# Kernel tuning notes

Measured on AMD Instinct MI355X. Metric: run time of the kernel, lower is better.

The kernel has to match this reference:

```python
import jax, jax.numpy as jnp
import numpy as np

N_NODES = 10000
N_EDGES = 128000


def _edge_conv(x, row, col, edge_attr, w1, b1, w2, b2):
    # gather endpoints, concat edge features, 2-layer MLP per edge
    m = jnp.concatenate([x[row], x[col], edge_attr], axis=1)  # [E, 2*in+edge]
    m = jax.nn.relu(m @ w1 + b1) @ w2 + b2                    # [E, out]
    # scatter-mean onto source nodes (flow='target_to_source' -> aggregate on row)
    n = x.shape[0]
    s = jax.ops.segment_sum(m, row, num_segments=n)
    cnt = jax.ops.segment_sum(jnp.ones((row.shape[0], 1), m.dtype), row, num_segments=n)
    out = s / jnp.maximum(cnt, 1.0)
    return out, m


def setup_inputs() -> dict:
    key = jax.random.key(0)
    ks = jax.random.split(key, 24)
    f = jnp.float32

    def lin(kw, kb, fan_in, fan_out):
        lim = 1.0 / np.sqrt(fan_in)
        w = jax.random.uniform(kw, (fan_in, fan_out), f, -lim, lim)
        b = jax.random.uniform(kb, (fan_out,), f, -lim, lim)
        return w, b

    inp = {}
    inp['x_org'] = jax.random.normal(ks[0], (N_NODES, 256), f)
    inp['x_rot'] = jax.random.normal(ks[1], (N_NODES, 4), f)
    inp['edge_index'] = jax.random.randint(ks[2], (2, N_EDGES), 0, N_NODES, jnp.int64 if jax.config.jax_enable_x64 else jnp.int32)
    inp['edge_attr'] = jax.random.normal(ks[3], (N_EDGES, 640), f)
    inp['edge_rot'] = jax.random.normal(ks[4], (N_EDGES, 4), f)

    # conv1: Linear(2*260+644=1164, 64), Linear(64, 64)
    inp['c1_w1'], inp['c1_b1'] = lin(ks[5], ks[6], 1164, 64)
    inp['c1_w2'], inp['c1_b2'] = lin(ks[7], ks[8], 64, 64)
    # conv2: Linear(2*64+704=832, 64), Linear(64, 64)
    inp['c2_w1'], inp['c2_b1'] = lin(ks[9], ks[10], 832, 64)
    inp['c2_w2'], inp['c2_b2'] = lin(ks[11], ks[12], 64, 64)
    # conv3: Linear(2*128+128=384, 64), Linear(64, 64)
    inp['c3_w1'], inp['c3_b1'] = lin(ks[13], ks[14], 384, 64)
    inp['c3_w2'], inp['c3_b2'] = lin(ks[15], ks[16], 64, 64)
    # conv4: Linear(384, 64), Linear(64, 64)
    inp['c4_w1'], inp['c4_b1'] = lin(ks[17], ks[18], 384, 64)
    inp['c4_w2'], inp['c4_b2'] = lin(ks[19], ks[20], 64, 64)
    # lin1: Linear(64, 4)
    inp['lin1_w'], inp['lin1_b'] = lin(ks[21], ks[22], 64, 4)
    # edge_fc: Linear(64, 32) -> ReLU -> Linear(32, 1)
    k23 = jax.random.split(ks[23], 4)
    inp['efc_w1'], inp['efc_b1'] = lin(k23[0], k23[1], 64, 32)
    inp['efc_w2'], inp['efc_b2'] = lin(k23[2], k23[3], 32, 1)
    return inp


def reference(x_org, x_rot, edge_index, edge_attr, edge_rot,
              c1_w1, c1_b1, c1_w2, c1_b2,
              c2_w1, c2_b1, c2_w2, c2_b2,
              c3_w1, c3_b1, c3_w2, c3_b2,
              c4_w1, c4_b1, c4_w2, c4_b2,
              lin1_w, lin1_b, efc_w1, efc_b1, efc_w2, efc_b2):
    node_feat = jnp.concatenate([x_org, x_rot], axis=1)
    edge_feat = jnp.concatenate([edge_attr, edge_rot], axis=1)
    row, col = edge_index[0], edge_index[1]
    E = edge_index.shape[1]

    x1, edge_x1 = _edge_conv(node_feat, row, col, edge_feat, c1_w1, c1_b1, c1_w2, c1_b2)
    edge_x1 = jax.nn.relu(edge_x1)

    x2, edge_x2 = _edge_conv(x1, row, col, jnp.concatenate([edge_attr, edge_x1], axis=1),
                             c2_w1, c2_b1, c2_w2, c2_b2)
    x2 = jax.nn.relu(x2)
    edge_x2 = jax.nn.relu(edge_x2)

    x3, edge_x3 = _edge_conv(jnp.concatenate([x2, x1], axis=1), row, col,
                             jnp.concatenate([edge_x2, edge_x1], axis=1),
                             c3_w1, c3_b1, c3_w2, c3_b2)
    x3 = jax.nn.relu(x3)
    edge_x3 = jax.nn.relu(edge_x3)

    x4, edge_x4 = _edge_conv(jnp.concatenate([x3, x2], axis=1), row, col,
                             jnp.concatenate([edge_x3, edge_x2], axis=1),
                             c4_w1, c4_b1, c4_w2, c4_b2)
    x4 = jax.nn.relu(x4)

    x = x4 @ lin1_w + lin1_b  # [N, 4]
    h = edge_x4[: E // 2] + edge_x4[E // 2:]
    pred_edge_res = jax.nn.relu(h @ efc_w1 + efc_b1) @ efc_w2 + efc_b2  # [E/2, 1]

    # F.normalize(x, p=2, dim=1)
    x = x / jnp.maximum(jnp.linalg.norm(x, axis=1, keepdims=True), 1e-12)
    return x, pred_edge_res
```

## Files before the change

### kernel.cpp

```cpp
#include <hip/hip_runtime.h>
#include <stdint.h>


#define N_NODES 10000
#define N_EDGES 128000
#define E_HALF  64000

typedef unsigned short u16;
constexpr int PAD = 18;

using bf16x8 = __attribute__((ext_vector_type(8))) short;
using f32x4  = __attribute__((ext_vector_type(4))) float;

#define MFMA16(A, B, C) C = __builtin_amdgcn_mfma_f32_16x16x32_bf16(A, B, C, 0, 0, 0)

__device__ __align__(256) float g_acc[N_NODES * 64];
__device__ __align__(256) float g_deg[N_NODES];
__device__ __align__(256) float g_P[N_NODES * 128];
__device__ __align__(256) float g_x1[N_NODES * 64];
__device__ __align__(256) float g_x2[N_NODES * 64];
__device__ __align__(256) float g_x3[N_NODES * 64];
__device__ __align__(256) float g_exA[(size_t)N_EDGES * 64];
__device__ __align__(256) float g_exB[(size_t)N_EDGES * 64];
__device__ __align__(256) u16  g_wpA_hi[11 * 4096];
__device__ __align__(256) u16  g_wpA_lo[11 * 4096];
__device__ __align__(256) u16  g_wp2_hi[4096];
__device__ __align__(256) u16  g_wp2_lo[4096];
__device__ __align__(256) int g_row[N_EDGES];
__device__ __align__(256) int g_col[N_EDGES];
__device__ int g_mode;
__device__ int g_is64;

__device__ __forceinline__ float b2f(u16 u) {
    return __uint_as_float(((unsigned int)u) << 16);
}
__device__ __forceinline__ u16 f2b(float f) {
    unsigned int u = __float_as_uint(f);
    u += 0x7FFFu + ((u >> 16) & 1u);
    return (u16)(u >> 16);
}
__device__ __forceinline__ float ldf(const u16* p)   { return b2f(*p); }
__device__ __forceinline__ float ldf(const float* p) { return *p; }
__device__ __forceinline__ void  stf(u16* p, float v)   { *p = f2b(v); }
__device__ __forceinline__ void  stf(float* p, float v) { *p = v; }

__device__ __forceinline__ float4 load4(const float* p) { return *(const float4*)p; }
__device__ __forceinline__ float4 load4(const u16* p) {
    ushort4 v = *(const ushort4*)p;
    return make_float4(b2f(v.x), b2f(v.y), b2f(v.z), b2f(v.w));
}

__device__ __forceinline__ void split_pack(float4 v, uint2& hi, uint2& lo) {
    unsigned int ux = __float_as_uint(v.x), uy = __float_as_uint(v.y);
    unsigned int uz = __float_as_uint(v.z), uw = __float_as_uint(v.w);
    unsigned int hx = ux & 0xFFFF0000u, hy = uy & 0xFFFF0000u;
    unsigned int hz = uz & 0xFFFF0000u, hw = uw & 0xFFFF0000u;
    hi.x = (hx >> 16) | hy;
    hi.y = (hz >> 16) | hw;
    u16 lx = f2b(v.x - __uint_as_float(hx));
    u16 ly = f2b(v.y - __uint_as_float(hy));
    u16 lz = f2b(v.z - __uint_as_float(hz));
    u16 lw = f2b(v.w - __uint_as_float(hw));
    lo.x = (unsigned int)lx | ((unsigned int)ly << 16);
    lo.y = (unsigned int)lz | ((unsigned int)lw << 16);
}

template<int K1, int K2> struct NGOff;
template<> struct NGOff<256, 4> { static constexpr size_t hi = (size_t)260 * 64; };
template<> struct NGOff<64, 0>  { static constexpr size_t hi = (size_t)64 * 64; };
template<> struct NGOff<64, 64> { static constexpr size_t hi = (size_t)128 * 64; };

template<int D>
__device__ __forceinline__ void stage_row(const u16* src, float* sm, int koff, int e, int t) {
    static_assert(D % 4 == 0, "D%4");
    for (int k = t * 4; k < D; k += 1024) {
        ushort4 v = *(const ushort4*)(src + k);
        sm[(koff + k + 0) * PAD + e] = b2f(v.x);
        sm[(koff + k + 1) * PAD + e] = b2f(v.y);
        sm[(koff + k + 2) * PAD + e] = b2f(v.z);
        sm[(koff + k + 3) * PAD + e] = b2f(v.w);
    }
}
template<int D>
__device__ __forceinline__ void stage_row(const float* src, float* sm, int koff, int e, int t) {
    static_assert(D % 4 == 0, "D%4");
    for (int k = t * 4; k < D; k += 1024) {
        float4 v = *(const float4*)(src + k);
        sm[(koff + k + 0) * PAD + e] = v.x;
        sm[(koff + k + 1) * PAD + e] = v.y;
        sm[(koff + k + 2) * PAD + e] = v.z;
        sm[(koff + k + 3) * PAD + e] = v.w;
    }
}

__global__ void detect_kernel(const void* x_org_v, const int* __restrict__ eidx) {
    const u16* w = (const u16*)x_org_v;
    const int t = threadIdx.x;
    int ok = 0;
    for (int i = t; i < 128; i += 64) {
        u16 v = w[i];
        int ex = (v >> 7) & 0xFF;
        ok += ((ex >= 0x68 && ex <= 0x88) || ((v & 0x7FFFu) == 0)) ? 1 : 0;
    }
    #pragma unroll
    for (int off = 32; off >= 1; off >>= 1) ok += __shfl_xor(ok, off);
    bool allz = true;
    for (int i = t; i < 2048; i += 64) allz = allz && (eidx[2 * i + 1] == 0);
    unsigned long long m = __ballot(allz);
    if (t == 0) {
        g_mode = (ok >= 110) ? 0 : 1;
        g_is64 = (m == ~0ull) ? 1 : 0;
    }
}

__global__ void cvt_idx(const int* __restrict__ eidx) {
    const int e = blockIdx.x * 256 + threadIdx.x;
    if (g_is64) {
        g_row[e] = eidx[2 * e];
        g_col[e] = eidx[2 * (e + N_EDGES)];
    } else {
        g_row[e] = eidx[e];
        g_col[e] = eidx[e + N_EDGES];
    }
}

__global__ void zero_all() {
    const int i = blockIdx.x * 256 + threadIdx.x;
    g_acc[i] = 0.f;
    if (i < N_NODES) g_deg[i] = 0.f;
}

__global__ void deg_kernel() {
    const int e = blockIdx.x * 256 + threadIdx.x;
    if (e < N_EDGES) atomicAdd(&g_deg[g_row[e]], 1.0f);
}

template<int K1, typename TA1, int K2, typename TA2, typename TW>
__device__ void node_gemm_body(float* sm, const TA1* A1, const TA2* A2,
                               const TW* Wbase, float* P) {
    constexpr int K = K1 + K2;
    const TW* Blo = Wbase;
    const TW* Bhi = Wbase + NGOff<K1, K2>::hi;
    const int t = threadIdx.x;
    const int c = t & 127;
    const int g = t >> 7;
    const int r0 = blockIdx.x * 16;
    for (int e = 0; e < 16; ++e) {
        stage_row<K1>(A1 + (size_t)(r0 + e) * K1, sm, 0, e, t);
        if constexpr (K2 > 0)
            stage_row<K2>(A2 + (size_t)(r0 + e) * K2, sm, K1, e, t);
    }
    __syncthreads();
    float acc[16];
    #pragma unroll
    for (int e = 0; e < 16; ++e) acc[e] = 0.f;
    const TW* Bp = (c < 64) ? (Blo + c) : (Bhi + (c - 64));
    const int kb = g * (K / 2), ke = kb + K / 2;
    for (int k = kb; k < ke; ++k) {
        float w = ldf(Bp + (size_t)k * 64);
        #pragma unroll
        for (int e = 0; e < 16; ++e) acc[e] += sm[k * PAD + e] * w;
    }
    __syncthreads();
    #pragma unroll
    for (int e = 0; e < 16; ++e) sm[(g * 16 + e) * 128 + c] = acc[e];
    __syncthreads();
    #pragma unroll
    for (int j = 0; j < 8; ++j) {
        int e = g * 8 + j;
        P[(size_t)(r0 + e) * 128 + c] = sm[e * 128 + c] + sm[(16 + e) * 128 + c];
    }
}

template<int K1, int K2>
__global__ void __launch_bounds__(256) node_gemm_in(
        const void* A1, const void* A2, const void* W, float* __restrict__ P) {
    extern __shared__ float sm[];
    if (g_mode == 0)
        node_gemm_body<K1, u16, K2, u16, u16>(sm, (const u16*)A1, (const u16*)A2,
                                              (const u16*)W, P);
    else
        node_gemm_body<K1, float, K2, float, float>(sm, (const float*)A1,
                                              (const float*)A2, (const float*)W, P);
}

template<int K1, int K2>
__global__ void __launch_bounds__(256) node_gemm_ws(
        const float* A1, const float* A2, const void* W, float* __restrict__ P) {
    extern __shared__ float sm[];
    if (g_mode == 0)
        node_gemm_body<K1, float, K2, float, u16>(sm, A1, A2, (const u16*)W, P);
    else
        node_gemm_body<K1, float, K2, float, float>(sm, A1, A2, (const float*)W, P);
}

template<typename TW>
__device__ void pack_w_body(const TW* w1, const TW* w2, int we, int ns) {
    const int idx = blockIdx.x * 256 + threadIdx.x;
    const int t1 = ns * 4096;
    if (idx < t1) {
        const int s = idx >> 12;
        const int rem = idx & 4095;
        const int kt = rem >> 11, ct = (rem >> 9) & 3, l = (rem >> 3) & 63, r = rem & 7;
        const int k = s * 64 + kt * 32 + 4 * (l >> 4) + (r & 3) + 16 * (r >> 2);
        const float v = ldf(w1 + (size_t)(we + k) * 64 + ct * 16 + (l & 15));
        const u16 hh = f2b(v);
        g_wpA_hi[idx] = hh;
        g_wpA_lo[idx] = f2b(v - b2f(hh));
    } else if (idx < t1 + 4096) {
        const int rem = idx - t1;
        const int kt = rem >> 11, ct = (rem >> 9) & 3, l = (rem >> 3) & 63, r = rem & 7;
        const int k = kt * 32 + 4 * (l >> 4) + (r & 3) + 16 * (r >> 2);
        const float v = ldf(w2 + (size_t)k * 64 + ct * 16 + (l & 15));
        const u16 hh = f2b(v);
        g_wp2_hi[rem] = hh;
        g_wp2_lo[rem] = f2b(v - b2f(hh));
    }
}
__global__ void pack_w_k(const void* w1, const void* w2, int we, int ns) {
    if (g_mode == 0) pack_w_body<u16>((const u16*)w1, (const u16*)w2, we, ns);
    else             pack_w_body<float>((const float*)w1, (const float*)w2, we, ns);
}

template<typename TA, typename TW, int NSA, int DB, bool RELU_OUT>
__device__ __forceinline__ void edge_mfma_body(
        u16* smA, int* srow, int* scol, float* b1s, float* b2s,
        float* rot, float* wtl,
        const TA* efa, const float* efb, const TA* rotsrc,
        const TW* w1, const TW* b1v, const TW* b2v, float* eout, int we) {
    constexpr int NS_TOT = NSA + (DB == 64 ? 1 : 0);
    const int t = threadIdx.x;
    const int lane = t & 63, wid = t >> 6;
    const int q = lane >> 4, n = lane & 15;
    const int e0 = blockIdx.x * 128;

    if (t < 128) srow[t] = g_row[e0 + t];
    else         scol[t - 128] = g_col[e0 + t - 128];
    if (t >= 128 && t < 192) b1s[t - 128] = ldf(b1v + (t - 128));
    if (t >= 192)            b2s[t - 192] = ldf(b2v + (t - 192));
    if constexpr (DB == 4) {
        if (t < 128) {
            float4 r4 = load4(rotsrc + (size_t)(e0 + t) * 4);
            rot[t * 4 + 0] = r4.x; rot[t * 4 + 1] = r4.y;
            rot[t * 4 + 2] = r4.z; rot[t * 4 + 3] = r4.w;
        }
        wtl[t] = ldf(w1 + (size_t)(we + NSA * 64 + (t >> 6)) * 64 + (t & 63));
    }

    f32x4 acc[2][4];
    #pragma unroll
    for (int a_ = 0; a_ < 2; ++a_)
        #pragma unroll
        for (int b_ = 0; b_ < 4; ++b_)
            acc[a_][b_] = (f32x4){0.f, 0.f, 0.f, 0.f};

    const int eb = t >> 4;
    const int cc = t & 15;

    for (int s = 0; s < NS_TOT; ++s) {
        #pragma unroll
        for (int p = 0; p < 8; ++p) {
            const int e = p * 16 + eb;
            float4 v;
            if (s < NSA) v = load4(efa + (size_t)(e0 + e) * (NSA * 64) + s * 64 + cc * 4);
            else         v = load4(efb + (size_t)(e0 + e) * 64 + cc * 4);
            uint2 hi, lo; split_pack(v, hi, lo);
            const int elem = (((cc >> 3) * 8 + (e >> 4)) * 64 + (cc & 3) * 16 + (e & 15)) * 8
                           + ((cc >> 2) & 1) * 4;
            *(uint2*)&smA[elem]        = hi;
            *(uint2*)&smA[elem + 8192] = lo;
        }
        __syncthreads();
        const u16* wph = g_wpA_hi + s * 4096;
        const u16* wpl = g_wpA_lo + s * 4096;
        #pragma unroll
        for (int kt = 0; kt < 2; ++kt) {
            const int r0 = ((kt * 8 + wid * 2 + 0) * 64 + lane) * 8;
            const int r1 = ((kt * 8 + wid * 2 + 1) * 64 + lane) * 8;
            bf16x8 ah0 = *(const bf16x8*)&smA[r0];
            bf16x8 ah1 = *(const bf16x8*)&smA[r1];
            bf16x8 al0 = *(const bf16x8*)&smA[r0 + 8192];
            bf16x8 al1 = *(const bf16x8*)&smA[r1 + 8192];
            #pragma unroll
            for (int ct = 0; ct < 4; ++ct) {
                bf16x8 bh = *(const bf16x8*)&wph[(kt * 4 + ct) * 512 + lane * 8];
                bf16x8 bl = *(const bf16x8*)&wpl[(kt * 4 + ct) * 512 + lane * 8];
                MFMA16(ah0, bh, acc[0][ct]);
                MFMA16(ah1, bh, acc[1][ct]);
                MFMA16(al0, bh, acc[0][ct]);
                MFMA16(al1, bh, acc[1][ct]);
                MFMA16(ah0, bl, acc[0][ct]);
                MFMA16(ah1, bl, acc[1][ct]);
            }
        }
        __syncthreads();
    }

    #pragma unroll
    for (int rt = 0; rt < 2; ++rt) {
        #pragma unroll
        for (int ct = 0; ct < 4; ++ct) {
            #pragma unroll
            for (int i = 0; i < 4; ++i) {
                const int rl = wid * 32 + rt * 16 + 4 * q + i;
                const int col = ct * 16 + n;
                float v = acc[rt][ct][i] + b1s[col]
                        + g_P[(size_t)srow[rl] * 128 + col]
                        + g_P[(size_t)scol[rl] * 128 + 64 + col];
                if constexpr (DB == 4) {
                    v += rot[rl * 4 + 0] * wtl[0 * 64 + col]
                       + rot[rl * 4 + 1] * wtl[1 * 64 + col]
                       + rot[rl * 4 + 2] * wtl[2 * 64 + col]
                       + rot[rl * 4 + 3] * wtl[3 * 64 + col];
                }
                v = fmaxf(v, 0.f);
                unsigned int hb = __float_as_uint(v) & 0xFFFF0000u;
                const u16 hh = (u16)(hb >> 16);
                const u16 hl = f2b(v - __uint_as_float(hb));
                const int off = wid * 4096
                              + (((ct >> 1) * 2 + rt) * 64 + (n >> 2) * 16 + 4 * q + i) * 8
                              + (ct & 1) * 4 + (n & 3);
                smA[off]        = hh;
                smA[off + 2048] = hl;
            }
        }
    }

    f32x4 oacc[2][4];
    #pragma unroll
    for (int rt = 0; rt < 2; ++rt)
        #pragma unroll
        for (int ct = 0; ct < 4; ++ct) {
            const float bb = b2s[ct * 16 + n];
            oacc[rt][ct] = (f32x4){bb, bb, bb, bb};
        }
    #pragma unroll
    for (int kt = 0; kt < 2; ++kt) {
        const int r0 = wid * 4096 + ((kt * 2 + 0) * 64 + lane) * 8;
        const int r1 = wid * 4096 + ((kt * 2 + 1) * 64 + lane) * 8;
        bf16x8 ah0 = *(const bf16x8*)&smA[r0];
        bf16x8 ah1 = *(const bf16x8*)&smA[r1];
        bf16x8 al0 = *(const bf16x8*)&smA[r0 + 2048];
        bf16x8 al1 = *(const bf16x8*)&smA[r1 + 2048];
        #pragma unroll
        for (int ct = 0; ct < 4; ++ct) {
            bf16x8 bh = *(const bf16x8*)&g_wp2_hi[(kt * 4 + ct) * 512 + lane * 8];
            bf16x8 bl = *(const bf16x8*)&g_wp2_lo[(kt * 4 + ct) * 512 + lane * 8];
            MFMA16(ah0, bh, oacc[0][ct]);
            MFMA16(ah1, bh, oacc[1][ct]);
            MFMA16(al0, bh, oacc[0][ct]);
            MFMA16(al1, bh, oacc[1][ct]);
            MFMA16(ah0, bl, oacc[0][ct]);
            MFMA16(ah1, bl, oacc[1][ct]);
        }
    }

    #pragma unroll
    for (int rt = 0; rt < 2; ++rt) {
        #pragma unroll
        for (int ct = 0; ct < 4; ++ct) {
            #pragma unroll
            for (int i = 0; i < 4; ++i) {
                const int rl = wid * 32 + rt * 16 + 4 * q + i;
                const int col = ct * 16 + n;
                const float v = oacc[rt][ct][i];
                atomicAdd(&g_acc[(size_t)srow[rl] * 64 + col], v);
                eout[(size_t)(e0 + rl) * 64 + col] = RELU_OUT ? fmaxf(v, 0.f) : v;
            }
        }
    }
}

template<int NSA, int DB, bool RELU_OUT>
__global__ void __launch_bounds__(256, 4) edge_mfma_in(
        const void* efa, const float* efb, const void* rotsrc,
        const void* w1, const void* b1, const void* b2, float* eout, int we) {
    __shared__ u16 smA[16384];
    __shared__ int srow[128], scol[128];
    __shared__ float b1s[64], b2s[64], rot[512], wtl[256];
    if (g_mode == 0)
        edge_mfma_body<u16, u16, NSA, DB, RELU_OUT>(smA, srow, scol, b1s, b2s, rot, wtl,
            (const u16*)efa, efb, (const u16*)rotsrc,
            (const u16*)w1, (const u16*)b1, (const u16*)b2, eout, we);
    else
        edge_mfma_body<float, float, NSA, DB, RELU_OUT>(smA, srow, scol, b1s, b2s, rot, wtl,
            (const float*)efa, efb, (const float*)rotsrc,
            (const float*)w1, (const float*)b1, (const float*)b2, eout, we);
}

template<int NSA, int DB, bool RELU_OUT>
__global__ void __launch_bounds__(256, 4) edge_mfma_ws(
        const float* efa, const float* efb,
        const void* w1, const void* b1, const void* b2, float* eout, int we) {
    __shared__ u16 smA[16384];
    __shared__ int srow[128], scol[128];
    __shared__ float b1s[64], b2s[64], rot[512], wtl[256];
    if (g_mode == 0)
        edge_mfma_body<float, u16, NSA, DB, RELU_OUT>(smA, srow, scol, b1s, b2s, rot, wtl,
            efa, efb, (const float*)nullptr,
            (const u16*)w1, (const u16*)b1, (const u16*)b2, eout, we);
    else
        edge_mfma_body<float, float, NSA, DB, RELU_OUT>(smA, srow, scol, b1s, b2s, rot, wtl,
            efa, efb, (const float*)nullptr,
            (const float*)w1, (const float*)b1, (const float*)b2, eout, we);
}

template<bool RELU>
__global__ void finalize_k(float* __restrict__ dst) {
    const int idx = blockIdx.x * 256 + threadIdx.x;
    float v = g_acc[idx] / fmaxf(g_deg[idx >> 6], 1.0f);
    g_acc[idx] = 0.f;
    if (RELU) v = fmaxf(v, 0.f);
    dst[idx] = v;
}

template<typename T>
__device__ void final_node_body(const T* w, const T* b, T* out) {
    const int t = threadIdx.x;
    const int lane = t & 63;
    const int n = blockIdx.x * 4 + (t >> 6);
    float inv = 1.0f / fmaxf(g_deg[n], 1.0f);
    float x4 = fmaxf(g_acc[(size_t)n * 64 + lane] * inv, 0.0f);
    float r[4];
    #pragma unroll
    for (int j = 0; j < 4; ++j) {
        float v = x4 * ldf(w + lane * 4 + j);
        #pragma unroll
        for (int off = 32; off >= 1; off >>= 1) v += __shfl_xor(v, off);
        r[j] = v + ldf(b + j);
    }
    float nrm = sqrtf(r[0]*r[0] + r[1]*r[1] + r[2]*r[2] + r[3]*r[3]);
    float dn = fmaxf(nrm, 1e-12f);
    if (lane < 4) stf(out + n * 4 + lane, r[lane] / dn);
}
__global__ void final_node(const void* w, const void* b, void* out) {
    if (g_mode == 0) final_node_body<u16>((const u16*)w, (const u16*)b, (u16*)out);
    else             final_node_body<float>((const float*)w, (const float*)b, (float*)out);
}

template<typename T>
__device__ void edge_head_body(const float* ex4, const T* w1, const T* b1,
                               const T* w2, const T* b2, T* out) {
    __shared__ float lw1[2048];
    __shared__ float lw2[32];
    const int t = threadIdx.x;
    for (int i = t; i < 2048; i += 256) lw1[i] = ldf(w1 + i);
    if (t < 32) lw2[t] = ldf(w2 + t);
    __syncthreads();
    const int e = blockIdx.x * 256 + t;
    float a[32];
    #pragma unroll
    for (int j = 0; j < 32; ++j) a[j] = ldf(b1 + j);
    const float* p0 = ex4 + (size_t)e * 64;
    const float* p1 = ex4 + (size_t)(e + E_HALF) * 64;
    for (int c = 0; c < 64; ++c) {
        float h = p0[c] + p1[c];
        #pragma unroll
        for (int j = 0; j < 32; ++j) a[j] += h * lw1[c * 32 + j];
    }
    float s = ldf(b2);
    #pragma unroll
    for (int j = 0; j < 32; ++j) s += fmaxf(a[j], 0.f) * lw2[j];
    stf(out + e, s);
}
__global__ void __launch_bounds__(256) edge_head(const float* ex4,
        const void* w1, const void* b1, const void* w2, const void* b2,
        void* out) {
    if (g_mode == 0)
        edge_head_body<u16>(ex4, (const u16*)w1, (const u16*)b1,
                            (const u16*)w2, (const u16*)b2, (u16*)out + 40000);
    else
        edge_head_body<float>(ex4, (const float*)w1, (const float*)b1,
                              (const float*)w2, (const float*)b2, (float*)out + 40000);
}

__global__ void sentinel_fill(unsigned int* out, int n_words) {
    int i = blockIdx.x * 256 + threadIdx.x;
    if (i < n_words) out[i] = 0x44794479u;
}

static void* sym_addr(const void* symbol) {
    void* p = nullptr;
    (void)hipGetSymbolAddress(&p, symbol);
    return p;
}

extern "C" void kernel_launch(void* const* d_in, const int* in_sizes, int n_in,
                              void* d_out, int out_size, void* d_ws, size_t ws_size,
                              hipStream_t stream) {
    (void)d_ws; (void)ws_size;
    bool ok = (n_in == 27) && (out_size == 104000)
           && (in_sizes[0] == 2560000) && (in_sizes[2] == 256000)
           && (in_sizes[3] == 81920000) && (in_sizes[5] == 74496)
           && (in_sizes[21] == 256) && (in_sizes[25] == 32);
    if (!ok) {
        sentinel_fill<<<204, 256, 0, stream>>>((unsigned int*)d_out, 52000);
        return;
    }
    const void* x_org     = d_in[0];
    const void* x_rot     = d_in[1];
    const int*  eidx      = (const int*)d_in[2];
    const void* edge_attr = d_in[3];
    const void* edge_rot  = d_in[4];

    float* P   = (float*)sym_addr(HIP_SYMBOL(g_P));
    float* x1  = (float*)sym_addr(HIP_SYMBOL(g_x1));
    float* x2  = (float*)sym_addr(HIP_SYMBOL(g_x2));
    float* x3  = (float*)sym_addr(HIP_SYMBOL(g_x3));
    float* exA = (float*)sym_addr(HIP_SYMBOL(g_exA));
    float* exB = (float*)sym_addr(HIP_SYMBOL(g_exB));

    detect_kernel<<<1, 64, 0, stream>>>(x_org, eidx);
    cvt_idx<<<500, 256, 0, stream>>>(eidx);
    zero_all<<<2500, 256, 0, stream>>>();
    deg_kernel<<<500, 256, 0, stream>>>();

    node_gemm_in<256, 4><<<625, 256, 18720, stream>>>(x_org, x_rot, d_in[5], P);
    pack_w_k<<<176, 256, 0, stream>>>(d_in[5], d_in[7], 520, 10);
    edge_mfma_in<10, 4, true><<<1000, 256, 0, stream>>>(
        edge_attr, nullptr, edge_rot, d_in[5], d_in[6], d_in[8], exA, 520);
    finalize_k<false><<<2500, 256, 0, stream>>>(x1);

    node_gemm_ws<64, 0><<<625, 256, 16384, stream>>>(x1, (const float*)nullptr,
                                                     d_in[9], P);
    pack_w_k<<<192, 256, 0, stream>>>(d_in[9], d_in[11], 128, 11);
    edge_mfma_in<10, 64, true><<<1000, 256, 0, stream>>>(
        edge_attr, exA, nullptr, d_in[9], d_in[10], d_in[12], exB, 128);
    finalize_k<true><<<2500, 256, 0, stream>>>(x2);

    node_gemm_ws<64, 64><<<625, 256, 16384, stream>>>(x2, x1, d_in[13], P);
    pack_w_k<<<48, 256, 0, stream>>>(d_in[13], d_in[15], 256, 2);
    edge_mfma_ws<1, 64, true><<<1000, 256, 0, stream>>>(
        exB, exA, d_in[13], d_in[14], d_in[16], exA, 256);
    finalize_k<true><<<2500, 256, 0, stream>>>(x3);

    node_gemm_ws<64, 64><<<625, 256, 16384, stream>>>(x3, x2, d_in[17], P);
    pack_w_k<<<48, 256, 0, stream>>>(d_in[17], d_in[19], 256, 2);
    edge_mfma_ws<1, 64, false><<<1000, 256, 0, stream>>>(
        exA, exB, d_in[17], d_in[18], d_in[20], exB, 256);

    final_node<<<2500, 256, 0, stream>>>(d_in[21], d_in[22], d_out);
    edge_head<<<250, 256, 0, stream>>>(exB, d_in[23], d_in[24], d_in[25], d_in[26],
                                       d_out);
}
```

Baseline: 969.4 us.

## Move node GEMMs to split-bf16 MFMA and swizzle edge LDS layout

Replaces the scalar FP32 per-node projection GEMM with an MFMA kernel that splits the activations and weights into hi/lo bf16 halves, using weights pre-packed by an extended pack kernel. The 4-wide rotation tail is handled in a small FP32 epilogue. It also applies an XOR swizzle to the shared-memory A tiles in both the node and edge MFMA kernels to reduce LDS bank conflicts. In exchange it adds a larger weight-packing pass and three-term bf16 precision emulation.

```diff
diff --git a/kernel.cpp b/kernel.cpp
--- a/kernel.cpp
+++ b/kernel.cpp
@@ -7,7 +7,6 @@
 #define E_HALF  64000
 
 typedef unsigned short u16;
-constexpr int PAD = 18;
 
 using bf16x8 = __attribute__((ext_vector_type(8))) short;
 using f32x4  = __attribute__((ext_vector_type(4))) float;
@@ -26,6 +25,8 @@
 __device__ __align__(256) u16  g_wpA_lo[11 * 4096];
 __device__ __align__(256) u16  g_wp2_hi[4096];
 __device__ __align__(256) u16  g_wp2_lo[4096];
+__device__ __align__(256) u16  g_wnp_hi[4 * 8192];
+__device__ __align__(256) u16  g_wnp_lo[4 * 8192];
 __device__ __align__(256) int g_row[N_EDGES];
 __device__ __align__(256) int g_col[N_EDGES];
 __device__ int g_mode;
@@ -48,6 +49,11 @@
 __device__ __forceinline__ float4 load4(const u16* p) {
     ushort4 v = *(const ushort4*)p;
     return make_float4(b2f(v.x), b2f(v.y), b2f(v.z), b2f(v.w));
+}
+
+template<int KTB>
+__device__ __forceinline__ int swz(int b) {
+    return b ^ ((b >> 4) & 3) ^ (((b >> KTB) & 1) << 2);
 }
 
 __device__ __forceinline__ void split_pack(float4 v, uint2& hi, uint2& lo) {
@@ -65,34 +71,6 @@
     lo.y = (unsigned int)lz | ((unsigned int)lw << 16);
 }
 
-template<int K1, int K2> struct NGOff;
-template<> struct NGOff<256, 4> { static constexpr size_t hi = (size_t)260 * 64; };
-template<> struct NGOff<64, 0>  { static constexpr size_t hi = (size_t)64 * 64; };
-template<> struct NGOff<64, 64> { static constexpr size_t hi = (size_t)128 * 64; };
-
-template<int D>
-__device__ __forceinline__ void stage_row(const u16* src, float* sm, int koff, int e, int t) {
-    static_assert(D % 4 == 0, "D%4");
-    for (int k = t * 4; k < D; k += 1024) {
-        ushort4 v = *(const ushort4*)(src + k);
-        sm[(koff + k + 0) * PAD + e] = b2f(v.x);
-        sm[(koff + k + 1) * PAD + e] = b2f(v.y);
-        sm[(koff + k + 2) * PAD + e] = b2f(v.z);
-        sm[(koff + k + 3) * PAD + e] = b2f(v.w);
-    }
-}
-template<int D>
-__device__ __forceinline__ void stage_row(const float* src, float* sm, int koff, int e, int t) {
-    static_assert(D % 4 == 0, "D%4");
-    for (int k = t * 4; k < D; k += 1024) {
-        float4 v = *(const float4*)(src + k);
-        sm[(koff + k + 0) * PAD + e] = v.x;
-        sm[(koff + k + 1) * PAD + e] = v.y;
-        sm[(koff + k + 2) * PAD + e] = v.z;
-        sm[(koff + k + 3) * PAD + e] = v.w;
-    }
-}
-
 __global__ void detect_kernel(const void* x_org_v, const int* __restrict__ eidx) {
     const u16* w = (const u16*)x_org_v;
     const int t = threadIdx.x;
@@ -135,67 +113,9 @@
     if (e < N_EDGES) atomicAdd(&g_deg[g_row[e]], 1.0f);
 }
 
-template<int K1, typename TA1, int K2, typename TA2, typename TW>
-__device__ void node_gemm_body(float* sm, const TA1* A1, const TA2* A2,
-                               const TW* Wbase, float* P) {
-    constexpr int K = K1 + K2;
-    const TW* Blo = Wbase;
-    const TW* Bhi = Wbase + NGOff<K1, K2>::hi;
-    const int t = threadIdx.x;
-    const int c = t & 127;
-    const int g = t >> 7;
-    const int r0 = blockIdx.x * 16;
-    for (int e = 0; e < 16; ++e) {
-        stage_row<K1>(A1 + (size_t)(r0 + e) * K1, sm, 0, e, t);
-        if constexpr (K2 > 0)
-            stage_row<K2>(A2 + (size_t)(r0 + e) * K2, sm, K1, e, t);
-    }
-    __syncthreads();
-    float acc[16];
-    #pragma unroll
-    for (int e = 0; e < 16; ++e) acc[e] = 0.f;
-    const TW* Bp = (c < 64) ? (Blo + c) : (Bhi + (c - 64));
-    const int kb = g * (K / 2), ke = kb + K / 2;
-    for (int k = kb; k < ke; ++k) {
-        float w = ldf(Bp + (size_t)k * 64);
-        #pragma unroll
-        for (int e = 0; e < 16; ++e) acc[e] += sm[k * PAD + e] * w;
-    }
-    __syncthreads();
-    #pragma unroll
-    for (int e = 0; e < 16; ++e) sm[(g * 16 + e) * 128 + c] = acc[e];
-    __syncthreads();
-    #pragma unroll
-    for (int j = 0; j < 8; ++j) {
-        int e = g * 8 + j;
-        P[(size_t)(r0 + e) * 128 + c] = sm[e * 128 + c] + sm[(16 + e) * 128 + c];
-    }
-}
-
-template<int K1, int K2>
-__global__ void __launch_bounds__(256) node_gemm_in(
-        const void* A1, const void* A2, const void* W, float* __restrict__ P) {
-    extern __shared__ float sm[];
-    if (g_mode == 0)
-        node_gemm_body<K1, u16, K2, u16, u16>(sm, (const u16*)A1, (const u16*)A2,
-                                              (const u16*)W, P);
-    else
-        node_gemm_body<K1, float, K2, float, float>(sm, (const float*)A1,
-                                              (const float*)A2, (const float*)W, P);
-}
-
-template<int K1, int K2>
-__global__ void __launch_bounds__(256) node_gemm_ws(
-        const float* A1, const float* A2, const void* W, float* __restrict__ P) {
-    extern __shared__ float sm[];
-    if (g_mode == 0)
-        node_gemm_body<K1, float, K2, float, u16>(sm, A1, A2, (const u16*)W, P);
-    else
-        node_gemm_body<K1, float, K2, float, float>(sm, A1, A2, (const float*)W, P);
-}
-
 template<typename TW>
-__device__ void pack_w_body(const TW* w1, const TW* w2, int we, int ns) {
+__device__ void pack_w_body(const TW* w1, const TW* w2, int we, int ns,
+                            int hioff, int nsn) {
     const int idx = blockIdx.x * 256 + threadIdx.x;
     const int t1 = ns * 4096;
     if (idx < t1) {
@@ -215,11 +135,130 @@
         const u16 hh = f2b(v);
         g_wp2_hi[rem] = hh;
         g_wp2_lo[rem] = f2b(v - b2f(hh));
-    }
-}
-__global__ void pack_w_k(const void* w1, const void* w2, int we, int ns) {
-    if (g_mode == 0) pack_w_body<u16>((const u16*)w1, (const u16*)w2, we, ns);
-    else             pack_w_body<float>((const float*)w1, (const float*)w2, we, ns);
+    } else if (idx < t1 + 4096 + nsn * 8192) {
+        const int rem = idx - t1 - 4096;
+        const int s = rem >> 13;
+        const int kt = (rem >> 12) & 1, ct = (rem >> 9) & 7, l = (rem >> 3) & 63, r = rem & 7;
+        const int k = s * 64 + kt * 32 + 4 * (l >> 4) + (r & 3) + 16 * (r >> 2);
+        const int col = ct * 16 + (l & 15);
+        const int row = (col < 64) ? k : (hioff + k);
+        const float v = ldf(w1 + (size_t)row * 64 + (col & 63));
+        const u16 hh = f2b(v);
+        g_wnp_hi[rem] = hh;
+        g_wnp_lo[rem] = f2b(v - b2f(hh));
+    }
+}
+__global__ void pack_w_k(const void* w1, const void* w2, int we, int ns,
+                         int hioff, int nsn) {
+    if (g_mode == 0) pack_w_body<u16>((const u16*)w1, (const u16*)w2, we, ns, hioff, nsn);
+    else             pack_w_body<float>((const float*)w1, (const float*)w2, we, ns, hioff, nsn);
+}
+
+template<typename TA, int NS1, int NS2, bool TAIL>
+__device__ void node_mfma_body(u16* smA, float* smrot, float* smwt,
+        const TA* A1, const float* A2, const TA* rotsrc, const TA* w1, float* P) {
+    constexpr int NS = NS1 + NS2;
+    const int t = threadIdx.x;
+    const int lane = t & 63, wid = t >> 6;
+    const int q = lane >> 4, n = lane & 15;
+    const int r0b = blockIdx.x * 64;
+
+    if constexpr (TAIL) {
+        if (t < 64) {
+            const int rr = min(r0b + t, N_NODES - 1);
+            float4 v = load4(rotsrc + (size_t)rr * 4);
+            smrot[t * 4 + 0] = v.x; smrot[t * 4 + 1] = v.y;
+            smrot[t * 4 + 2] = v.z; smrot[t * 4 + 3] = v.w;
+        }
+        for (int i = t; i < 512; i += 256) {
+            const int j = i >> 7, c = i & 127;
+            const int row = (c < 64) ? (256 + j) : (516 + j);
+            smwt[i] = ldf(w1 + (size_t)row * 64 + (c & 63));
+        }
+    }
+
+    f32x4 acc[8];
+    #pragma unroll
+    for (int ct = 0; ct < 8; ++ct) acc[ct] = (f32x4){0.f, 0.f, 0.f, 0.f};
+
+    const int eb = t >> 4;
+    const int cc = t & 15;
+
+    for (int s = 0; s < NS; ++s) {
+        #pragma unroll
+        for (int p = 0; p < 4; ++p) {
+            const int e = p * 16 + eb;
+            const int row = min(r0b + e, N_NODES - 1);
+            float4 v;
+            if constexpr (NS2 > 0)
+                v = (s < NS1) ? load4(A1 + (size_t)row * (NS1 * 64) + s * 64 + cc * 4)
+                              : load4(A2 + (size_t)row * (NS2 * 64) + (s - NS1) * 64 + cc * 4);
+            else
+                v = load4(A1 + (size_t)row * (NS1 * 64) + s * 64 + cc * 4);
+            uint2 hi, lo; split_pack(v, hi, lo);
+            const int blk = ((cc >> 3) * 4 + (e >> 4)) * 64 + (cc & 3) * 16 + (e & 15);
+            const int elem = swz<8>(blk) * 8 + ((cc >> 2) & 1) * 4;
+            *(uint2*)&smA[elem]        = hi;
+            *(uint2*)&smA[elem + 4096] = lo;
+        }
+        __syncthreads();
+        const u16* wph = g_wnp_hi + s * 8192;
+        const u16* wpl = g_wnp_lo + s * 8192;
+        #pragma unroll
+        for (int kt = 0; kt < 2; ++kt) {
+            const int ad = swz<8>((kt * 4 + wid) * 64 + lane) * 8;
+            bf16x8 ah = *(const bf16x8*)&smA[ad];
+            bf16x8 al = *(const bf16x8*)&smA[ad + 4096];
+            #pragma unroll
+            for (int ct = 0; ct < 8; ++ct) {
+                bf16x8 bh = *(const bf16x8*)&wph[(kt * 8 + ct) * 512 + lane * 8];
+                bf16x8 bl = *(const bf16x8*)&wpl[(kt * 8 + ct) * 512 + lane * 8];
+                MFMA16(ah, bh, acc[ct]);
+                MFMA16(al, bh, acc[ct]);
+                MFMA16(ah, bl, acc[ct]);
+            }
+        }
+        __syncthreads();
+    }
+
+    #pragma unroll
+    for (int ct = 0; ct < 8; ++ct) {
+        #pragma unroll
+        for (int i = 0; i < 4; ++i) {
+            const int rl = wid * 16 + 4 * q + i;
+            const int row = r0b + rl;
+            const int col = ct * 16 + n;
+            float v = acc[ct][i];
+            if constexpr (TAIL)
+                v += smrot[rl * 4 + 0] * smwt[0 * 128 + col]
+                   + smrot[rl * 4 + 1] * smwt[1 * 128 + col]
+                   + smrot[rl * 4 + 2] * smwt[2 * 128 + col]
+                   + smrot[rl * 4 + 3] * smwt[3 * 128 + col];
+            if (row < N_NODES) P[(size_t)row * 128 + col] = v;
+        }
+    }
+}
+
+template<int NS1, bool TAIL>
+__global__ void __launch_bounds__(256) node_mfma_in(
+        const void* A1, const void* rotsrc, const void* w1, float* __restrict__ P) {
+    __shared__ u16 smA[8192];
+    __shared__ float smrot[256], smwt[512];
+    if (g_mode == 0)
+        node_mfma_body<u16, NS1, 0, TAIL>(smA, smrot, smwt, (const u16*)A1,
+            nullptr, (const u16*)rotsrc, (const u16*)w1, P);
+    else
+        node_mfma_body<float, NS1, 0, TAIL>(smA, smrot, smwt, (const float*)A1,
+            nullptr, (const float*)rotsrc, (const float*)w1, P);
+}
+
+template<int NS1, int NS2>
+__global__ void __launch_bounds__(256) node_mfma_ws(
+        const float* A1, const float* A2, float* __restrict__ P) {
+    __shared__ u16 smA[8192];
+    __shared__ float smrot[256], smwt[512];
+    node_mfma_body<float, NS1, NS2, false>(smA, smrot, smwt, A1, A2,
+        (const float*)nullptr, (const float*)nullptr, P);
 }
 
 template<typename TA, typename TW, int NSA, int DB, bool RELU_OUT>
@@ -265,8 +304,8 @@
             if (s < NSA) v = load4(efa + (size_t)(e0 + e) * (NSA * 64) + s * 64 + cc * 4);
             else         v = load4(efb + (size_t)(e0 + e) * 64 + cc * 4);
             uint2 hi, lo; split_pack(v, hi, lo);
-            const int elem = (((cc >> 3) * 8 + (e >> 4)) * 64 + (cc & 3) * 16 + (e & 15)) * 8
-                           + ((cc >> 2) & 1) * 4;
+            const int blk = ((cc >> 3) * 8 + (e >> 4)) * 64 + (cc & 3) * 16 + (e & 15);
+            const int elem = swz<9>(blk) * 8 + ((cc >> 2) & 1) * 4;
             *(uint2*)&smA[elem]        = hi;
             *(uint2*)&smA[elem + 8192] = lo;
         }
@@ -275,8 +314,10 @@
         const u16* wpl = g_wpA_lo + s * 4096;
         #pragma unroll
         for (int kt = 0; kt < 2; ++kt) {
-            const int r0 = ((kt * 8 + wid * 2 + 0) * 64 + lane) * 8;
-            const int r1 = ((kt * 8 + wid * 2 + 1) * 64 + lane) * 8;
+            const int b0 = (kt * 8 + wid * 2 + 0) * 64 + lane;
+            const int b1 = (kt * 8 + wid * 2 + 1) * 64 + lane;
+            const int r0 = swz<9>(b0) * 8;
+            const int r1 = swz<9>(b1) * 8;
             bf16x8 ah0 = *(const bf16x8*)&smA[r0];
             bf16x8 ah1 = *(const bf16x8*)&smA[r1];
             bf16x8 al0 = *(const bf16x8*)&smA[r0 + 8192];
@@ -515,27 +556,26 @@
     zero_all<<<2500, 256, 0, stream>>>();
     deg_kernel<<<500, 256, 0, stream>>>();
 
-    node_gemm_in<256, 4><<<625, 256, 18720, stream>>>(x_org, x_rot, d_in[5], P);
-    pack_w_k<<<176, 256, 0, stream>>>(d_in[5], d_in[7], 520, 10);
+    pack_w_k<<<304, 256, 0, stream>>>(d_in[5], d_in[7], 520, 10, 260, 4);
+    node_mfma_in<4, true><<<157, 256, 0, stream>>>(x_org, x_rot, d_in[5], P);
     edge_mfma_in<10, 4, true><<<1000, 256, 0, stream>>>(
         edge_attr, nullptr, edge_rot, d_in[5], d_in[6], d_in[8], exA, 520);
     finalize_k<false><<<2500, 256, 0, stream>>>(x1);
 
-    node_gemm_ws<64, 0><<<625, 256, 16384, stream>>>(x1, (const float*)nullptr,
-                                                     d_in[9], P);
-    pack_w_k<<<192, 256, 0, stream>>>(d_in[9], d_in[11], 128, 11);
+    pack_w_k<<<224, 256, 0, stream>>>(d_in[9], d_in[11], 128, 11, 64, 1);
+    node_mfma_ws<1, 0><<<157, 256, 0, stream>>>(x1, nullptr, P);
     edge_mfma_in<10, 64, true><<<1000, 256, 0, stream>>>(
         edge_attr, exA, nullptr, d_in[9], d_in[10], d_in[12], exB, 128);
     finalize_k<true><<<2500, 256, 0, stream>>>(x2);
 
-    node_gemm_ws<64, 64><<<625, 256, 16384, stream>>>(x2, x1, d_in[13], P);
-    pack_w_k<<<48, 256, 0, stream>>>(d_in[13], d_in[15], 256, 2);
+    pack_w_k<<<112, 256, 0, stream>>>(d_in[13], d_in[15], 256, 2, 128, 2);
+    node_mfma_ws<1, 1><<<157, 256, 0, stream>>>(x2, x1, P);
     edge_mfma_ws<1, 64, true><<<1000, 256, 0, stream>>>(
         exB, exA, d_in[13], d_in[14], d_in[16], exA, 256);
     finalize_k<true><<<2500, 256, 0, stream>>>(x3);
 
-    node_gemm_ws<64, 64><<<625, 256, 16384, stream>>>(x3, x2, d_in[17], P);
-    pack_w_k<<<48, 256, 0, stream>>>(d_in[17], d_in[19], 256, 2);
+    pack_w_k<<<112, 256, 0, stream>>>(d_in[17], d_in[19], 256, 2, 128, 2);
+    node_mfma_ws<1, 1><<<157, 256, 0, stream>>>(x3, x2, P);
     edge_mfma_ws<1, 64, false><<<1000, 256, 0, stream>>>(
         exA, exB, d_in[17], d_in[18], d_in[20], exB, 256);
 
```

New measurement: 922.8 us. -4.8%, faster.
